# Optimization experiments

Hardware: AMD Instinct MI355X
Metric: run time of the kernel (lower is better)

## Reference

```python
import jax, jax.numpy as jnp
import numpy as np

B = 65536      # batch
FDIM = 256     # features_dim (flatten extractor => obs dim)
ADIM = 8       # action dim
T = 3          # n_tasks
H = 256        # net_arch width
IN = FDIM + ADIM

_PARAM_SHAPES = [("W1", (T, IN, H)), ("b1", (T, H)), ("W2", (T, H, H)), ("b2", (T, H)),
                 ("W3", (T, H, H)), ("b3", (T, H)), ("W4", (T, H, 1)), ("b4", (T, 1))]

def setup_inputs() -> dict:
    key = jax.random.key(0)
    ks = jax.random.split(key, 2 + 2 * len(_PARAM_SHAPES))
    d = {"obs": jax.random.normal(ks[0], (B, FDIM), dtype=jnp.float32),
         "actions": jax.random.normal(ks[1], (B, ADIM), dtype=jnp.float32)}
    i = 2
    for q in ("q1", "q2"):
        for name, sh in _PARAM_SHAPES:
            d[f"{q}_{name}"] = jax.random.normal(ks[i], sh, dtype=jnp.float32) * 0.05
            i += 1
    return d

def _heads(x, W1, b1, W2, b2, W3, b3, W4, b4):
    # x: [B, IN]; per-task stacked MLP -> [T, B]
    h = jax.nn.relu(jnp.einsum('bi,tih->tbh', x, W1) + b1[:, None, :])
    h = jax.nn.relu(jnp.einsum('tbh,thk->tbk', h, W2) + b2[:, None, :])
    h = jax.nn.relu(jnp.einsum('tbh,thk->tbk', h, W3) + b3[:, None, :])
    return (jnp.einsum('tbh,tho->tbo', h, W4) + b4[:, None, :])[..., 0]

def reference(obs, actions,
              q1_W1, q1_b1, q1_W2, q1_b2, q1_W3, q1_b3, q1_W4, q1_b4,
              q2_W1, q2_b1, q2_W2, q2_b2, q2_W3, q2_b3, q2_W4, q2_b4):
    x = jnp.concatenate([obs, actions], axis=1)           # [B, IN]
    task = jnp.argmax(obs[:, -T:], axis=-1)               # [B] hard top-1 routing
    mask = jax.nn.one_hot(task, T, dtype=x.dtype).T       # [T, B]
    y1 = _heads(x, q1_W1, q1_b1, q1_W2, q1_b2, q1_W3, q1_b3, q1_W4, q1_b4)  # [T, B]
    y2 = _heads(x, q2_W1, q2_b1, q2_W2, q2_b2, q2_W3, q2_b3, q2_W4, q2_b4)
    q1 = jnp.sum(y1 * mask, axis=0)[:, None]              # [B, 1]
    q2 = jnp.sum(y2 * mask, axis=0)[:, None]
    return (q1, q2)
```

## Files before the change

kernel.cpp:

```cpp
#include <hip/hip_runtime.h>
#include <hip/hip_bf16.h>


#define NB 65536
#define MROWS 48
#define XSTR 296
#define HSTR 264

typedef __attribute__((ext_vector_type(8))) short short8;
typedef __attribute__((ext_vector_type(4))) short short4v;
typedef __attribute__((ext_vector_type(4))) float f32x4;

__device__ __forceinline__ float bf2f(unsigned short u){
  union { unsigned int i; float f; } x; x.i = ((unsigned int)u) << 16; return x.f;
}
__device__ __forceinline__ unsigned short f2bf(float f){
  unsigned int x = __float_as_uint(f);
  x += 0x7fffu + ((x >> 16) & 1u);
  return (unsigned short)(x >> 16);
}
__device__ __forceinline__ float ldval(const void* p, int idx, int isbf16){
  return isbf16 ? bf2f(((const unsigned short*)p)[idx]) : ((const float*)p)[idx];
}

__device__ __forceinline__ int block_sniff(const void* obs, int tid, int* sflag){
  if (tid < 64) {
    unsigned short u = ((const unsigned short*)obs)[tid * 2];
    int e = (u >> 7) & 0xFF;
    unsigned long long m = __ballot(e >= 110 && e <= 132);
    if (tid == 0) *sflag = (__popcll(m) >= 32) ? 1 : 0;
  }
  __syncthreads();
  return *sflag;
}

struct KParams {
  const void* obs;
  const void* act;
  const unsigned short* w1t[2];
  const unsigned short* w2t[2];
  const unsigned short* w3t[2];
  const void* b1[2];
  const void* b2[2];
  const void* b3[2];
  const void* w4[2];
  const void* b4[2];
  const int* counts;
  const int* perm;
  void* out;
};

__device__ __forceinline__ int task_of(const void* obs, int b, int isbf16){
  float v0, v1, v2;
  if (isbf16) {
    short4v u = *(const short4v*)((const unsigned short*)obs + b * 256 + 252);
    v0 = bf2f((unsigned short)u[1]); v1 = bf2f((unsigned short)u[2]); v2 = bf2f((unsigned short)u[3]);
  } else {
    f32x4 u = *(const f32x4*)((const float*)obs + b * 256 + 252);
    v0 = u[1]; v1 = u[2]; v2 = u[3];
  }
  int t = 0; float m = v0;
  if (v1 > m) { m = v1; t = 1; }
  if (v2 > m) { t = 2; }
  return t;
}

__global__ void prep_count(const void* q1W1, const void* q1W2, const void* q1W3,
                           const void* q2W1, const void* q2W2, const void* q2W3,
                           const void* obs, unsigned short* out,
                           int* hist, unsigned char* tasks){
  __shared__ int sflag;
  int tid = threadIdx.x;
  int isbf16 = block_sniff(obs, tid, &sflag);
  if (blockIdx.x >= 600) {
    __shared__ int h[3];
    if (tid < 3) h[tid] = 0;
    __syncthreads();
    int blk = blockIdx.x - 600;
    int b = blk * 256 + tid;
    int t = task_of(obs, b, isbf16);
    tasks[b] = (unsigned char)t;
    atomicAdd(&h[t], 1);
    __syncthreads();
    if (tid < 3) hist[blk * 3 + tid] = h[tid];
    return;
  }
  int gid8 = (blockIdx.x * 256 + tid) * 8;
  int net = gid8 / 614400;
  int idx = gid8 - net * 614400;
  const void* W1 = net ? q2W1 : q1W1;
  const void* W2 = net ? q2W2 : q1W2;
  const void* W3 = net ? q2W3 : q1W3;
  short8 sv;
  if (idx < 221184) {
    int t = idx / 73728; int i = idx - t * 73728;
    int g = i / 4608;  int r = i - g * 4608;
    int kb = r >> 9;   int q2 = r & 511;
    int l16 = q2 >> 5; int rem = q2 & 31;
    int n = g * 16 + l16;
    int k = kb * 32 + (rem & ~7);
    #pragma unroll
    for (int j = 0; j < 8; j++) {
      int kk = k + j;
      sv[j] = (kk < 264) ? (short)f2bf(ldval(W1, (t * 264 + kk) * 256 + n, isbf16)) : (short)0;
    }
  } else if (idx < 417792) {
    int j0 = idx - 221184;
    int t = j0 >> 16; int i = j0 & 65535;
    int g = i >> 12;  int r = i & 4095;
    int kb = r >> 9;  int q2 = r & 511;
    int l16 = q2 >> 5; int rem = q2 & 31;
    int n = g * 16 + l16;
    int k = kb * 32 + (rem & ~7);
    #pragma unroll
    for (int j = 0; j < 8; j++)
      sv[j] = (short)f2bf(ldval(W2, t * 65536 + (k + j) * 256 + n, isbf16));
  } else {
    int j0 = idx - 417792;
    int t = j0 >> 16; int i = j0 & 65535;
    int g = i >> 12;  int r = i & 4095;
    int kb = r >> 9;  int q2 = r & 511;
    int l16 = q2 >> 5; int rem = q2 & 31;
    int n = g * 16 + l16;
    int k = kb * 32 + (rem & ~7);
    #pragma unroll
    for (int j = 0; j < 8; j++)
      sv[j] = (short)f2bf(ldval(W3, t * 65536 + (k + j) * 256 + n, isbf16));
  }
  *(short8*)(out + net * 614400 + idx) = sv;
}

__global__ void route_scatter(const unsigned char* __restrict__ tasks,
                              const int* __restrict__ hist,
                              int* counts, int* perm){
  __shared__ int sh[3][256];
  __shared__ int totals[3], pres[3], base[3], zz[3];
  int tid = threadIdx.x;
  int blk = blockIdx.x;
  sh[0][tid] = hist[tid * 3 + 0];
  sh[1][tid] = hist[tid * 3 + 1];
  sh[2][tid] = hist[tid * 3 + 2];
  if (tid < 3) zz[tid] = 0;
  __syncthreads();
  if (tid < 3) {
    int tot = 0, pre = 0;
    for (int b = 0; b < 256; b++) {
      int v = sh[tid][b];
      if (b < blk) pre += v;
      tot += v;
    }
    totals[tid] = tot; pres[tid] = pre;
  }
  __syncthreads();
  if (tid < 3) {
    int a0 = ((totals[0] + MROWS - 1) / MROWS) * MROWS;
    int a1 = ((totals[1] + MROWS - 1) / MROWS) * MROWS;
    int off = (tid == 0) ? 0 : (tid == 1) ? a0 : a0 + a1;
    base[tid] = off + pres[tid];
    if (blk == 0) counts[tid] = totals[tid];
  }
  __syncthreads();
  int b = blk * 256 + tid;
  int t = tasks[b];
  int r = atomicAdd(&zz[t], 1);
  perm[base[t] + r] = b;
}

template<int KC>
__device__ __forceinline__ void run_layer(const unsigned short* __restrict__ lin, int lstride,
                                          const unsigned short* __restrict__ wt,
                                          const void* bias, unsigned short* lout,
                                          int isbf16, int wave, int quad, int l16, int nbase){
  const unsigned short* wg = wt + (wave * 2) * (KC * 512) + l16 * 32 + quad * 8;
  short8 bfr[KC][2];
  #pragma unroll
  for (int kb = 0; kb < KC; ++kb) {
    bfr[kb][0] = *(const short8*)(wg + kb * 512);
    bfr[kb][1] = *(const short8*)(wg + KC * 512 + kb * 512);
  }
  f32x4 acc[3][2] = {};
  #pragma unroll
  for (int kb = 0; kb < KC; ++kb) {
    short8 afr[3];
    int ko = kb * 32 + quad * 8;
    #pragma unroll
    for (int mt = 0; mt < 3; mt++)
      afr[mt] = *(const short8*)(lin + (mt * 16 + l16) * lstride + ko);
    #pragma unroll
    for (int mt = 0; mt < 3; mt++)
      #pragma unroll
      for (int nt = 0; nt < 2; nt++)
        acc[mt][nt] = __builtin_amdgcn_mfma_f32_16x16x32_bf16(afr[mt], bfr[kb][nt], acc[mt][nt], 0, 0, 0);
  }
  float bv[2];
  #pragma unroll
  for (int nt = 0; nt < 2; nt++) bv[nt] = ldval(bias, nbase + nt * 16 + l16, isbf16);
  #pragma unroll
  for (int mt = 0; mt < 3; mt++)
    #pragma unroll
    for (int nt = 0; nt < 2; nt++) {
      f32x4 a = acc[mt][nt];
      #pragma unroll
      for (int r = 0; r < 4; r++) {
        float v = fmaxf(a[r] + bv[nt], 0.f);
        lout[(mt * 16 + quad * 4 + r) * HSTR + nbase + nt * 16 + l16] = f2bf(v);
      }
    }
  __syncthreads();
}

__global__ __launch_bounds__(512, 6) void fused_kernel(KParams p){
  __shared__ unsigned short X[MROWS * XSTR];
  __shared__ unsigned short HA[MROWS * HSTR];
  unsigned short* HB = X;
  int* sflag = (int*)HA;

  int tid = threadIdx.x;
  int net = blockIdx.y;
  int p0  = blockIdx.x * MROWS;
  int isbf16 = block_sniff(p.obs, tid, sflag);
  int c0 = p.counts[0], c1 = p.counts[1], c2 = p.counts[2];
  int off1 = ((c0 + MROWS - 1) / MROWS) * MROWS;
  int off2 = off1 + ((c1 + MROWS - 1) / MROWS) * MROWS;
  int task  = (p0 >= off2) ? 2 : ((p0 >= off1) ? 1 : 0);
  int segend = (task == 0) ? c0 : (task == 1) ? off1 + c1 : off2 + c2;

  if (tid < MROWS * 8) {
    int srow = tid >> 3, seg = tid & 7;
    int pos = p0 + srow;
    int r = (pos < segend) ? p.perm[pos] : -1;
    #pragma unroll
    for (int j = 0; j < 5; ++j) {
      int c = seg + 8 * j;
      if (c <= 35) {
        short8 sv = {0,0,0,0,0,0,0,0};
        if (r >= 0 && c < 33) {
          if (isbf16) {
            const unsigned short* src = (c < 32) ? ((const unsigned short*)p.obs + r * 256 + c * 8)
                                                 : ((const unsigned short*)p.act + r * 8);
            sv = *(const short8*)src;
          } else {
            const float* src = (c < 32) ? ((const float*)p.obs + r * 256 + c * 8)
                                        : ((const float*)p.act + r * 8);
            f32x4 a = *(const f32x4*)src;
            f32x4 b = *(const f32x4*)(src + 4);
            #pragma unroll
            for (int q = 0; q < 4; q++) { sv[q] = (short)f2bf(a[q]); sv[4 + q] = (short)f2bf(b[q]); }
          }
        }
        *(short8*)(X + srow * XSTR + c * 8) = sv;
      }
    }
  }
  __syncthreads();

  int wave = tid >> 6, lane = tid & 63, quad = lane >> 4, l16 = lane & 15;
  int nbase = wave * 32;

  int bsz = isbf16 ? 2 : 4;
  run_layer<9>(X,  XSTR, p.w1t[net] + task * 73728, (const char*)p.b1[net] + task * 256 * bsz, HA, isbf16, wave, quad, l16, nbase);
  run_layer<8>(HA, HSTR, p.w2t[net] + task * 65536, (const char*)p.b2[net] + task * 256 * bsz, HB, isbf16, wave, quad, l16, nbase);
  run_layer<8>(HB, HSTR, p.w3t[net] + task * 65536, (const char*)p.b3[net] + task * 256 * bsz, HA, isbf16, wave, quad, l16, nbase);

  if (tid < MROWS * 8) {
    int row = tid >> 3, seg = tid & 7;
    float s = 0.f;
    #pragma unroll
    for (int kk = 0; kk < 32; kk += 8) {
      short8 hv = *(const short8*)(HA + row * HSTR + seg * 32 + kk);
      float wv[8];
      if (isbf16) {
        const unsigned short* w4p = (const unsigned short*)p.w4[net] + task * 256 + seg * 32 + kk;
        short8 t = *(const short8*)w4p;
        #pragma unroll
        for (int j = 0; j < 8; j++) wv[j] = bf2f((unsigned short)t[j]);
      } else {
        const float* w4p = (const float*)p.w4[net] + task * 256 + seg * 32 + kk;
        f32x4 a = *(const f32x4*)w4p;
        f32x4 b = *(const f32x4*)(w4p + 4);
        #pragma unroll
        for (int j = 0; j < 4; j++) { wv[j] = a[j]; wv[4 + j] = b[j]; }
      }
      #pragma unroll
      for (int j = 0; j < 8; j++)
        s += bf2f((unsigned short)hv[j]) * wv[j];
    }
    s += __shfl_xor(s, 1);
    s += __shfl_xor(s, 2);
    s += __shfl_xor(s, 4);
    if (seg == 0) {
      int pos = p0 + row;
      if (pos < segend) {
        int r = p.perm[pos];
        float y = s + ldval(p.b4[net], task, isbf16);
        if (isbf16) ((unsigned short*)p.out)[net * NB + r] = f2bf(y);
        else        ((float*)p.out)[net * NB + r] = y;
      }
    }
  }
}

extern "C" void kernel_launch(void* const* d_in, const int* in_sizes, int n_in,
                              void* d_out, int out_size, void* d_ws, size_t ws_size,
                              hipStream_t stream) {
  char* ws = (char*)d_ws;
  int* counts  = (int*)ws;
  int* hist    = (int*)(ws + 64);
  unsigned char* tasks = (unsigned char*)(ws + 3200);
  int* perm    = (int*)(ws + 68800);
  unsigned short* wts  = (unsigned short*)(ws + 331520);

  const void* obs = d_in[0];
  const void* act = d_in[1];

  prep_count<<<856, 256, 0, stream>>>(d_in[2], d_in[4], d_in[6],
                                      d_in[10], d_in[12], d_in[14],
                                      obs, wts, hist, tasks);
  route_scatter<<<256, 256, 0, stream>>>(tasks, hist, counts, perm);

  KParams kp;
  kp.obs = obs; kp.act = act;
  for (int q = 0; q < 2; q++) {
    int base = 2 + q * 8;
    kp.b1[q] = d_in[base + 1];
    kp.b2[q] = d_in[base + 3];
    kp.b3[q] = d_in[base + 5];
    kp.w4[q] = d_in[base + 6];
    kp.b4[q] = d_in[base + 7];
    kp.w1t[q] = wts + q * 614400;
    kp.w2t[q] = wts + q * 614400 + 221184;
    kp.w3t[q] = wts + q * 614400 + 417792;
  }
  kp.counts = counts; kp.perm = perm;
  kp.out = d_out;

  fused_kernel<<<dim3(1368, 2), 512, 0, stream>>>(kp);
}
```

Before: 222.0 us.

## Process both Q-networks in one block sharing the gathered input tile

Each block now handles 32 rows for both networks, four waves per network, and gathers the input tile once instead of once per network on a separate grid dimension. Each wave computes a 32x64 output tile and streams weight fragments from global memory per k-step, where before it held a 48x32 tile's weights preloaded in registers. This halves input gathering and routing work and raises MFMA work per A-fragment load. In exchange it re-reads weights more often, uses more LDS per block (separate hidden buffers per network), and lowers launch bounds occupancy from 6 to 4.

```diff
diff --git a/kernel.cpp b/kernel.cpp
--- a/kernel.cpp
+++ b/kernel.cpp
@@ -3,7 +3,7 @@
 
 
 #define NB 65536
-#define MROWS 48
+#define MROWS 32
 #define XSTR 296
 #define HSTR 264
 
@@ -170,35 +170,32 @@
 __device__ __forceinline__ void run_layer(const unsigned short* __restrict__ lin, int lstride,
                                           const unsigned short* __restrict__ wt,
                                           const void* bias, unsigned short* lout,
-                                          int isbf16, int wave, int quad, int l16, int nbase){
-  const unsigned short* wg = wt + (wave * 2) * (KC * 512) + l16 * 32 + quad * 8;
-  short8 bfr[KC][2];
+                                          int isbf16, int quad, int l16, int nbase){
+  const unsigned short* wg = wt + (nbase >> 4) * (KC * 512) + l16 * 32 + quad * 8;
+  f32x4 acc[2][4] = {};
   #pragma unroll
   for (int kb = 0; kb < KC; ++kb) {
-    bfr[kb][0] = *(const short8*)(wg + kb * 512);
-    bfr[kb][1] = *(const short8*)(wg + KC * 512 + kb * 512);
-  }
-  f32x4 acc[3][2] = {};
+    short8 bfr[4], afr[2];
+    #pragma unroll
+    for (int nt = 0; nt < 4; nt++)
+      bfr[nt] = *(const short8*)(wg + nt * (KC * 512) + kb * 512);
+    int ko = kb * 32 + quad * 8;
+    #pragma unroll
+    for (int mt = 0; mt < 2; mt++)
+      afr[mt] = *(const short8*)(lin + (mt * 16 + l16) * lstride + ko);
+    #pragma unroll
+    for (int mt = 0; mt < 2; mt++)
+      #pragma unroll
+      for (int nt = 0; nt < 4; nt++)
+        acc[mt][nt] = __builtin_amdgcn_mfma_f32_16x16x32_bf16(afr[mt], bfr[nt], acc[mt][nt], 0, 0, 0);
+  }
+  float bv[4];
   #pragma unroll
-  for (int kb = 0; kb < KC; ++kb) {
-    short8 afr[3];
-    int ko = kb * 32 + quad * 8;
-    #pragma unroll
-    for (int mt = 0; mt < 3; mt++)
-      afr[mt] = *(const short8*)(lin + (mt * 16 + l16) * lstride + ko);
-    #pragma unroll
-    for (int mt = 0; mt < 3; mt++)
-      #pragma unroll
-      for (int nt = 0; nt < 2; nt++)
-        acc[mt][nt] = __builtin_amdgcn_mfma_f32_16x16x32_bf16(afr[mt], bfr[kb][nt], acc[mt][nt], 0, 0, 0);
-  }
-  float bv[2];
+  for (int nt = 0; nt < 4; nt++) bv[nt] = ldval(bias, nbase + nt * 16 + l16, isbf16);
   #pragma unroll
-  for (int nt = 0; nt < 2; nt++) bv[nt] = ldval(bias, nbase + nt * 16 + l16, isbf16);
-  #pragma unroll
-  for (int mt = 0; mt < 3; mt++)
-    #pragma unroll
-    for (int nt = 0; nt < 2; nt++) {
+  for (int mt = 0; mt < 2; mt++)
+    #pragma unroll
+    for (int nt = 0; nt < 4; nt++) {
       f32x4 a = acc[mt][nt];
       #pragma unroll
       for (int r = 0; r < 4; r++) {
@@ -209,14 +206,13 @@
   __syncthreads();
 }
 
-__global__ __launch_bounds__(512, 6) void fused_kernel(KParams p){
+__global__ __launch_bounds__(512, 4) void fused_kernel(KParams p){
   __shared__ unsigned short X[MROWS * XSTR];
-  __shared__ unsigned short HA[MROWS * HSTR];
-  unsigned short* HB = X;
-  int* sflag = (int*)HA;
+  __shared__ unsigned short H1[2][MROWS * HSTR];
+  __shared__ unsigned short H2b[MROWS * HSTR];
+  int* sflag = (int*)H1;
 
   int tid = threadIdx.x;
-  int net = blockIdx.y;
   int p0  = blockIdx.x * MROWS;
   int isbf16 = block_sniff(p.obs, tid, sflag);
   int c0 = p.counts[0], c1 = p.counts[1], c2 = p.counts[2];
@@ -225,13 +221,13 @@
   int task  = (p0 >= off2) ? 2 : ((p0 >= off1) ? 1 : 0);
   int segend = (task == 0) ? c0 : (task == 1) ? off1 + c1 : off2 + c2;
 
-  if (tid < MROWS * 8) {
-    int srow = tid >> 3, seg = tid & 7;
+  {
+    int srow = tid >> 4, seg = tid & 15;
     int pos = p0 + srow;
     int r = (pos < segend) ? p.perm[pos] : -1;
     #pragma unroll
-    for (int j = 0; j < 5; ++j) {
-      int c = seg + 8 * j;
+    for (int j = 0; j < 3; ++j) {
+      int c = seg + 16 * j;
       if (c <= 35) {
         short8 sv = {0,0,0,0,0,0,0,0};
         if (r >= 0 && c < 33) {
@@ -255,27 +251,30 @@
   __syncthreads();
 
   int wave = tid >> 6, lane = tid & 63, quad = lane >> 4, l16 = lane & 15;
-  int nbase = wave * 32;
-
+  int net  = wave >> 2;
+  int nbase = (wave & 3) * 64;
+
+  unsigned short* HB = net ? H2b : X;
   int bsz = isbf16 ? 2 : 4;
-  run_layer<9>(X,  XSTR, p.w1t[net] + task * 73728, (const char*)p.b1[net] + task * 256 * bsz, HA, isbf16, wave, quad, l16, nbase);
-  run_layer<8>(HA, HSTR, p.w2t[net] + task * 65536, (const char*)p.b2[net] + task * 256 * bsz, HB, isbf16, wave, quad, l16, nbase);
-  run_layer<8>(HB, HSTR, p.w3t[net] + task * 65536, (const char*)p.b3[net] + task * 256 * bsz, HA, isbf16, wave, quad, l16, nbase);
-
-  if (tid < MROWS * 8) {
-    int row = tid >> 3, seg = tid & 7;
+  run_layer<9>(X,       XSTR, p.w1t[net] + task * 73728, (const char*)p.b1[net] + task * 256 * bsz, H1[net], isbf16, quad, l16, nbase);
+  run_layer<8>(H1[net], HSTR, p.w2t[net] + task * 65536, (const char*)p.b2[net] + task * 256 * bsz, HB,      isbf16, quad, l16, nbase);
+  run_layer<8>(HB,      HSTR, p.w3t[net] + task * 65536, (const char*)p.b3[net] + task * 256 * bsz, H1[net], isbf16, quad, l16, nbase);
+
+  {
+    int onet = tid >> 8, row = (tid >> 3) & 31, seg = tid & 7;
+    const unsigned short* h3 = H1[onet];
     float s = 0.f;
     #pragma unroll
     for (int kk = 0; kk < 32; kk += 8) {
-      short8 hv = *(const short8*)(HA + row * HSTR + seg * 32 + kk);
+      short8 hv = *(const short8*)(h3 + row * HSTR + seg * 32 + kk);
       float wv[8];
       if (isbf16) {
-        const unsigned short* w4p = (const unsigned short*)p.w4[net] + task * 256 + seg * 32 + kk;
+        const unsigned short* w4p = (const unsigned short*)p.w4[onet] + task * 256 + seg * 32 + kk;
         short8 t = *(const short8*)w4p;
         #pragma unroll
         for (int j = 0; j < 8; j++) wv[j] = bf2f((unsigned short)t[j]);
       } else {
-        const float* w4p = (const float*)p.w4[net] + task * 256 + seg * 32 + kk;
+        const float* w4p = (const float*)p.w4[onet] + task * 256 + seg * 32 + kk;
         f32x4 a = *(const f32x4*)w4p;
         f32x4 b = *(const f32x4*)(w4p + 4);
         #pragma unroll
@@ -292,9 +291,9 @@
       int pos = p0 + row;
       if (pos < segend) {
         int r = p.perm[pos];
-        float y = s + ldval(p.b4[net], task, isbf16);
-        if (isbf16) ((unsigned short*)p.out)[net * NB + r] = f2bf(y);
-        else        ((float*)p.out)[net * NB + r] = y;
+        float y = s + ldval(p.b4[onet], task, isbf16);
+        if (isbf16) ((unsigned short*)p.out)[onet * NB + r] = f2bf(y);
+        else        ((float*)p.out)[onet * NB + r] = y;
       }
     }
   }
@@ -334,5 +333,5 @@
   kp.counts = counts; kp.perm = perm;
   kp.out = d_out;
 
-  fused_kernel<<<dim3(1368, 2), 512, 0, stream>>>(kp);
-}
+  fused_kernel<<<2050, 512, 0, stream>>>(kp);
+}
```

After: 261.9 us. 18.0% more time.
